# Optimization experiments

Hardware: AMD Instinct MI355X
Metric: run time of the kernel (lower is better)

Reference implementation:

```python
import jax, jax.numpy as jnp
import numpy as np

N = 100000      # nodes
E = 3200000     # edges (avg degree 32)
NFEAT = 512
HID = 64
NCLASS = 64
ALPHA = 0.1
NITER = 10


def setup_inputs() -> dict:
    key = jax.random.key(0)
    k1, k2, k3, k4, k5 = jax.random.split(key, 5)
    x = jax.random.normal(k1, (N, NFEAT), dtype=jnp.float32)
    edge_index = jax.random.randint(k2, (2, E), 0, N, dtype=jnp.int32)
    edge_weight = jax.random.uniform(k3, (E,), dtype=jnp.float32)
    W1 = jax.random.normal(k4, (NFEAT, HID), dtype=jnp.float32) * 0.05
    W2 = jax.random.normal(k5, (HID, NCLASS), dtype=jnp.float32) * 0.05
    return {"x": x, "edge_index": edge_index, "edge_weight": edge_weight,
            "W1": W1, "W2": W2}


def reference(x, edge_index, edge_weight, W1, W2):
    # _transform_features (eval mode: dropout = identity, bias=False)
    h = jax.nn.relu(x @ W1)            # [N, HID]
    z0 = h @ W2                        # [N, NCLASS]
    src = edge_index[0]
    dst = edge_index[1]
    z = z0
    # APPNP power iteration: z = adj @ z + alpha * z0
    for _ in range(NITER):
        msg = edge_weight[:, None] * z[src]                          # [E, NCLASS]
        z = jax.ops.segment_sum(msg, dst, num_segments=N) + ALPHA * z0
    return jax.nn.log_softmax(z, axis=-1)
```

## Files before the change

### kernel.cpp

```cpp
#include <hip/hip_runtime.h>

#define NN     100000
#define EE     3200000
#define NF     512
#define HIDN   64
#define NCLS   64
#define ALPHA  0.1f

#define CHUNK  512
#define NB     196

typedef unsigned short ushort_t;
typedef unsigned int   uint_t;

__device__ inline ushort_t f2bf(float f)
{
    uint_t u = __float_as_uint(f);
    u += 0x7FFFu + ((u >> 16) & 1u);
    return (ushort_t)(u >> 16);
}
__device__ inline float bf2f(ushort_t b)
{
    return __uint_as_float(((uint_t)b) << 16);
}

template <bool RELU>
__global__ __launch_bounds__(256) void gemm_kernel(
    const float* __restrict__ A, const float* __restrict__ B,
    float* __restrict__ C, int nrows, int K)
{
    const int BK = 16;
    __shared__ float AsT[BK][68];
    __shared__ float Bs [BK][68];

    int tid = threadIdx.x;
    int tx  = tid & 15;
    int ty  = tid >> 4;
    int rowBase = blockIdx.x * 64;

    int arow = tid >> 2;
    int ak   = (tid & 3) * 4;
    int brow = tid >> 4;
    int bcol = (tid & 15) * 4;

    float acc[4][4] = {};

    for (int k0 = 0; k0 < K; k0 += BK) {
        float4 av;
        int gr = rowBase + arow;
        if (gr < nrows) av = *(const float4*)(A + (size_t)gr * K + k0 + ak);
        else            av = make_float4(0.f, 0.f, 0.f, 0.f);
        float4 bv = *(const float4*)(B + (size_t)(k0 + brow) * 64 + bcol);

        __syncthreads();
        AsT[ak + 0][arow] = av.x;
        AsT[ak + 1][arow] = av.y;
        AsT[ak + 2][arow] = av.z;
        AsT[ak + 3][arow] = av.w;
        *(float4*)&Bs[brow][bcol] = bv;
        __syncthreads();

#pragma unroll
        for (int kk = 0; kk < BK; ++kk) {
            float4 a = *(const float4*)&AsT[kk][ty * 4];
            float4 b = *(const float4*)&Bs [kk][tx * 4];
            acc[0][0] = fmaf(a.x, b.x, acc[0][0]);
            acc[0][1] = fmaf(a.x, b.y, acc[0][1]);
            acc[0][2] = fmaf(a.x, b.z, acc[0][2]);
            acc[0][3] = fmaf(a.x, b.w, acc[0][3]);
            acc[1][0] = fmaf(a.y, b.x, acc[1][0]);
            acc[1][1] = fmaf(a.y, b.y, acc[1][1]);
            acc[1][2] = fmaf(a.y, b.z, acc[1][2]);
            acc[1][3] = fmaf(a.y, b.w, acc[1][3]);
            acc[2][0] = fmaf(a.z, b.x, acc[2][0]);
            acc[2][1] = fmaf(a.z, b.y, acc[2][1]);
            acc[2][2] = fmaf(a.z, b.z, acc[2][2]);
            acc[2][3] = fmaf(a.z, b.w, acc[2][3]);
            acc[3][0] = fmaf(a.w, b.x, acc[3][0]);
            acc[3][1] = fmaf(a.w, b.y, acc[3][1]);
            acc[3][2] = fmaf(a.w, b.z, acc[3][2]);
            acc[3][3] = fmaf(a.w, b.w, acc[3][3]);
        }
    }

#pragma unroll
    for (int i = 0; i < 4; ++i) {
        int r = rowBase + ty * 4 + i;
        if (r < nrows) {
            float4 o;
            o.x = acc[i][0]; o.y = acc[i][1]; o.z = acc[i][2]; o.w = acc[i][3];
            if (RELU) {
                o.x = fmaxf(o.x, 0.f); o.y = fmaxf(o.y, 0.f);
                o.z = fmaxf(o.z, 0.f); o.w = fmaxf(o.w, 0.f);
            }
            *(float4*)(C + (size_t)r * 64 + tx * 4) = o;
        }
    }
}

__global__ __launch_bounds__(256) void zero_kernel(int* __restrict__ p, int n)
{
    int i = blockIdx.x * 256 + threadIdx.x;
    if (i < n) p[i] = 0;
}

__global__ __launch_bounds__(256) void count_kernel(const int* __restrict__ dst,
                                                    int* __restrict__ deg)
{
    int e = blockIdx.x * 256 + threadIdx.x;
    if (e < EE) atomicAdd(&deg[dst[e]], 1);
}

__global__ __launch_bounds__(256) void scanA_kernel(const int* __restrict__ deg,
                                                    int* __restrict__ bsum)
{
    int b = blockIdx.x, t = threadIdx.x;
    int i = b * CHUNK + t * 2;
    int v = 0;
    if (i < NN)     v += deg[i];
    if (i + 1 < NN) v += deg[i + 1];
    __shared__ int sm[256];
    sm[t] = v;
    __syncthreads();
    for (int o = 128; o > 0; o >>= 1) {
        if (t < o) sm[t] += sm[t + o];
        __syncthreads();
    }
    if (t == 0) bsum[b] = sm[0];
}

__global__ __launch_bounds__(256) void scanB_kernel(const int* __restrict__ bsum,
                                                    int* __restrict__ bbase,
                                                    int* __restrict__ offs)
{
    int t = threadIdx.x;
    int v = (t < NB) ? bsum[t] : 0;
    __shared__ int sm[256];
    sm[t] = v;
    __syncthreads();
    for (int o = 1; o < 256; o <<= 1) {
        int u = (t >= o) ? sm[t - o] : 0;
        __syncthreads();
        sm[t] += u;
        __syncthreads();
    }
    if (t < NB) bbase[t] = sm[t] - v;
    if (t == 0) offs[NN] = EE;
}

__global__ __launch_bounds__(256) void scanC_kernel(const int* __restrict__ deg,
                                                    const int* __restrict__ bbase,
                                                    int* __restrict__ offs,
                                                    int* __restrict__ cursor)
{
    int b = blockIdx.x, t = threadIdx.x;
    int i0 = b * CHUNK + t * 2;
    int d0 = (i0 < NN)     ? deg[i0]     : 0;
    int d1 = (i0 + 1 < NN) ? deg[i0 + 1] : 0;
    int local = d0 + d1;
    __shared__ int sm[256];
    sm[t] = local;
    __syncthreads();
    for (int o = 1; o < 256; o <<= 1) {
        int u = (t >= o) ? sm[t - o] : 0;
        __syncthreads();
        sm[t] += u;
        __syncthreads();
    }
    int excl = sm[t] - local + bbase[b];
    if (i0 < NN)     { offs[i0]     = excl;      cursor[i0]     = excl;      }
    if (i0 + 1 < NN) { offs[i0 + 1] = excl + d0; cursor[i0 + 1] = excl + d0; }
}

__global__ __launch_bounds__(256) void scatter_kernel(
    const int* __restrict__ src, const int* __restrict__ dst,
    const float* __restrict__ w, int* cursor, int2* __restrict__ csr)
{
    int e = blockIdx.x * 256 + threadIdx.x;
    if (e >= EE) return;
    int d = dst[e];
    int pos = atomicAdd(&cursor[d], 1);
    csr[pos] = make_int2(src[e], __float_as_int(w[e]));
}

__global__ __launch_bounds__(256) void cvt_kernel(const float* __restrict__ z0,
                                                  ushort_t* __restrict__ zb)
{
    int i = (blockIdx.x * 256 + threadIdx.x) * 4;
    if (i >= NN * 64) return;
    float4 v = *(const float4*)(z0 + i);
    ushort4 o;
    o.x = f2bf(v.x); o.y = f2bf(v.y); o.z = f2bf(v.z); o.w = f2bf(v.w);
    *(ushort4*)(zb + i) = o;
}

template <bool LSM>
__global__ __launch_bounds__(256) void propagate_kernel(
    const ushort_t* __restrict__ zin, const float* __restrict__ z0,
    ushort_t* __restrict__ zout_b, float* __restrict__ zout_f,
    const int* __restrict__ offs, const int2* __restrict__ csr)
{
    int gid  = blockIdx.x * 256 + threadIdx.x;
    int node = gid >> 6;
    int lane = gid & 63;
    if (node >= NN) return;

    int beg = offs[node];
    int end = offs[node + 1];
    float acc = 0.f;
    int j = beg;
    for (; j + 8 <= end; j += 8) {
        int2 e0 = csr[j],     e1 = csr[j + 1], e2 = csr[j + 2], e3 = csr[j + 3];
        int2 e4 = csr[j + 4], e5 = csr[j + 5], e6 = csr[j + 6], e7 = csr[j + 7];
        float v0 = bf2f(zin[(size_t)e0.x * 64 + lane]);
        float v1 = bf2f(zin[(size_t)e1.x * 64 + lane]);
        float v2 = bf2f(zin[(size_t)e2.x * 64 + lane]);
        float v3 = bf2f(zin[(size_t)e3.x * 64 + lane]);
        float v4 = bf2f(zin[(size_t)e4.x * 64 + lane]);
        float v5 = bf2f(zin[(size_t)e5.x * 64 + lane]);
        float v6 = bf2f(zin[(size_t)e6.x * 64 + lane]);
        float v7 = bf2f(zin[(size_t)e7.x * 64 + lane]);
        acc = fmaf(__int_as_float(e0.y), v0, acc);
        acc = fmaf(__int_as_float(e1.y), v1, acc);
        acc = fmaf(__int_as_float(e2.y), v2, acc);
        acc = fmaf(__int_as_float(e3.y), v3, acc);
        acc = fmaf(__int_as_float(e4.y), v4, acc);
        acc = fmaf(__int_as_float(e5.y), v5, acc);
        acc = fmaf(__int_as_float(e6.y), v6, acc);
        acc = fmaf(__int_as_float(e7.y), v7, acc);
    }
    for (; j < end; ++j) {
        int2 e = csr[j];
        acc = fmaf(__int_as_float(e.y), bf2f(zin[(size_t)e.x * 64 + lane]), acc);
    }

    float out = fmaf(ALPHA, z0[(size_t)node * 64 + lane], acc);

    if (LSM) {
        float m = out;
#pragma unroll
        for (int o = 32; o > 0; o >>= 1) m = fmaxf(m, __shfl_xor(m, o, 64));
        float e = __expf(out - m);
        float s = e;
#pragma unroll
        for (int o = 32; o > 0; o >>= 1) s += __shfl_xor(s, o, 64);
        zout_f[(size_t)node * 64 + lane] = (out - m) - __logf(s);
    } else {
        zout_b[(size_t)node * 64 + lane] = f2bf(out);
    }
}

extern "C" void kernel_launch(void* const* d_in, const int* in_sizes, int n_in,
                              void* d_out, int out_size, void* d_ws, size_t ws_size,
                              hipStream_t stream)
{
    const float* x  = (const float*)d_in[0];
    const int*   ei = (const int*)  d_in[1];
    const float* ew = (const float*)d_in[2];
    const float* W1 = (const float*)d_in[3];
    const float* W2 = (const float*)d_in[4];
    const int* src = ei;
    const int* dst = ei + EE;

    char* ws = (char*)d_ws;
    size_t off = 0;
    auto alloc = [&](size_t bytes) -> char* {
        char* p = ws + off;
        off += (bytes + 255) & ~(size_t)255;
        return p;
    };

    float*    h     = (float*)   alloc((size_t)NN * HIDN * 4);
    float*    z0    = (float*)   alloc((size_t)NN * NCLS * 4);
    ushort_t* zbA   = (ushort_t*)alloc((size_t)NN * NCLS * 2);
    ushort_t* zbB   = (ushort_t*)alloc((size_t)NN * NCLS * 2);
    int*      deg   = (int*)     alloc((size_t)NN * 4);
    int*      offs  = (int*)     alloc((size_t)(NN + 1) * 4);
    int*      cur_  = (int*)     alloc((size_t)NN * 4);
    int*      bsum  = (int*)     alloc((size_t)NB * 4);
    int*      bbase = (int*)     alloc((size_t)NB * 4);

    int2* csr = (int2*)h;

    gemm_kernel<true ><<<(NN + 63) / 64, 256, 0, stream>>>(x, W1, h, NN, NF);
    gemm_kernel<false><<<(NN + 63) / 64, 256, 0, stream>>>(h, W2, z0, NN, HIDN);

    zero_kernel<<<(NN + 255) / 256, 256, 0, stream>>>(deg, NN);
    count_kernel<<<EE / 256, 256, 0, stream>>>(dst, deg);
    scanA_kernel<<<NB, 256, 0, stream>>>(deg, bsum);
    scanB_kernel<<<1, 256, 0, stream>>>(bsum, bbase, offs);
    scanC_kernel<<<NB, 256, 0, stream>>>(deg, bbase, offs, cur_);
    scatter_kernel<<<EE / 256, 256, 0, stream>>>(src, dst, ew, cur_, csr);

    cvt_kernel<<<(NN * 64 / 4 + 255) / 256, 256, 0, stream>>>(z0, zbA);

    const ushort_t* cur = zbA;
    ushort_t* nxt = zbB;
    for (int it = 0; it < 9; ++it) {
        propagate_kernel<false><<<(NN * 64) / 256, 256, 0, stream>>>(
            cur, z0, nxt, nullptr, offs, csr);
        ushort_t* t = (ushort_t*)cur; cur = nxt; nxt = t;
    }
    propagate_kernel<true><<<(NN * 64) / 256, 256, 0, stream>>>(
        cur, z0, nullptr, (float*)d_out, offs, csr);
}
```

Measured before the change: 1.610 ms.

## Fuse bf16 conversion into GEMM2, store alpha*z0 in bf16, partition scatter, nontemporal loads

The second GEMM now writes bf16 z0 and a precomputed bf16 alpha*z0 directly, which removes the separate conversion kernel and the fp32 z0 buffer. Each propagate pass therefore reads half the bytes for the residual term. The scatter kernel is restructured so each block handles one of 8 destination-node ranges, grouping atomics and CSR writes into smaller regions for locality. CSR edge loads and output stores use nontemporal hints. Rounding alpha*z0 to bf16 adds a little precision loss, and the scatter now reads dst eight times over.

```diff
diff --git a/kernel.cpp b/kernel.cpp
--- a/kernel.cpp
+++ b/kernel.cpp
@@ -10,6 +10,8 @@
 #define CHUNK  512
 #define NB     196
 
+#define SC_BLOCKS 2048
+
 typedef unsigned short ushort_t;
 typedef unsigned int   uint_t;
 
@@ -22,6 +24,16 @@
 __device__ inline float bf2f(ushort_t b)
 {
     return __uint_as_float(((uint_t)b) << 16);
+}
+
+__device__ inline int2 ldnt_e(const int2* p)
+{
+    unsigned long long v =
+        __builtin_nontemporal_load((const unsigned long long*)p);
+    int2 r;
+    r.x = (int)(v & 0xFFFFFFFFull);
+    r.y = (int)(v >> 32);
+    return r;
 }
 
 template <bool RELU>
@@ -98,6 +110,79 @@
     }
 }
 
+__global__ __launch_bounds__(256) void gemm2_kernel(
+    const float* __restrict__ A, const float* __restrict__ B,
+    ushort_t* __restrict__ zb, ushort_t* __restrict__ az, int nrows, int K)
+{
+    const int BK = 16;
+    __shared__ float AsT[BK][68];
+    __shared__ float Bs [BK][68];
+
+    int tid = threadIdx.x;
+    int tx  = tid & 15;
+    int ty  = tid >> 4;
+    int rowBase = blockIdx.x * 64;
+
+    int arow = tid >> 2;
+    int ak   = (tid & 3) * 4;
+    int brow = tid >> 4;
+    int bcol = (tid & 15) * 4;
+
+    float acc[4][4] = {};
+
+    for (int k0 = 0; k0 < K; k0 += BK) {
+        float4 av;
+        int gr = rowBase + arow;
+        if (gr < nrows) av = *(const float4*)(A + (size_t)gr * K + k0 + ak);
+        else            av = make_float4(0.f, 0.f, 0.f, 0.f);
+        float4 bv = *(const float4*)(B + (size_t)(k0 + brow) * 64 + bcol);
+
+        __syncthreads();
+        AsT[ak + 0][arow] = av.x;
+        AsT[ak + 1][arow] = av.y;
+        AsT[ak + 2][arow] = av.z;
+        AsT[ak + 3][arow] = av.w;
+        *(float4*)&Bs[brow][bcol] = bv;
+        __syncthreads();
+
+#pragma unroll
+        for (int kk = 0; kk < BK; ++kk) {
+            float4 a = *(const float4*)&AsT[kk][ty * 4];
+            float4 b = *(const float4*)&Bs [kk][tx * 4];
+            acc[0][0] = fmaf(a.x, b.x, acc[0][0]);
+            acc[0][1] = fmaf(a.x, b.y, acc[0][1]);
+            acc[0][2] = fmaf(a.x, b.z, acc[0][2]);
+            acc[0][3] = fmaf(a.x, b.w, acc[0][3]);
+            acc[1][0] = fmaf(a.y, b.x, acc[1][0]);
+            acc[1][1] = fmaf(a.y, b.y, acc[1][1]);
+            acc[1][2] = fmaf(a.y, b.z, acc[1][2]);
+            acc[1][3] = fmaf(a.y, b.w, acc[1][3]);
+            acc[2][0] = fmaf(a.z, b.x, acc[2][0]);
+            acc[2][1] = fmaf(a.z, b.y, acc[2][1]);
+            acc[2][2] = fmaf(a.z, b.z, acc[2][2]);
+            acc[2][3] = fmaf(a.z, b.w, acc[2][3]);
+            acc[3][0] = fmaf(a.w, b.x, acc[3][0]);
+            acc[3][1] = fmaf(a.w, b.y, acc[3][1]);
+            acc[3][2] = fmaf(a.w, b.z, acc[3][2]);
+            acc[3][3] = fmaf(a.w, b.w, acc[3][3]);
+        }
+    }
+
+#pragma unroll
+    for (int i = 0; i < 4; ++i) {
+        int r = rowBase + ty * 4 + i;
+        if (r < nrows) {
+            ushort4 o, oa;
+            o.x  = f2bf(acc[i][0]);         o.y  = f2bf(acc[i][1]);
+            o.z  = f2bf(acc[i][2]);         o.w  = f2bf(acc[i][3]);
+            oa.x = f2bf(ALPHA * acc[i][0]); oa.y = f2bf(ALPHA * acc[i][1]);
+            oa.z = f2bf(ALPHA * acc[i][2]); oa.w = f2bf(ALPHA * acc[i][3]);
+            *(ushort4*)(zb + (size_t)r * 64 + tx * 4) = o;
+            *(ushort4*)(az + (size_t)r * 64 + tx * 4) = oa;
+        }
+    }
+}
+
 __global__ __launch_bounds__(256) void zero_kernel(int* __restrict__ p, int n)
 {
     int i = blockIdx.x * 256 + threadIdx.x;
@@ -176,27 +261,23 @@
     const int* __restrict__ src, const int* __restrict__ dst,
     const float* __restrict__ w, int* cursor, int2* __restrict__ csr)
 {
-    int e = blockIdx.x * 256 + threadIdx.x;
-    if (e >= EE) return;
-    int d = dst[e];
-    int pos = atomicAdd(&cursor[d], 1);
-    csr[pos] = make_int2(src[e], __float_as_int(w[e]));
-}
-
-__global__ __launch_bounds__(256) void cvt_kernel(const float* __restrict__ z0,
-                                                  ushort_t* __restrict__ zb)
-{
-    int i = (blockIdx.x * 256 + threadIdx.x) * 4;
-    if (i >= NN * 64) return;
-    float4 v = *(const float4*)(z0 + i);
-    ushort4 o;
-    o.x = f2bf(v.x); o.y = f2bf(v.y); o.z = f2bf(v.z); o.w = f2bf(v.w);
-    *(ushort4*)(zb + i) = o;
+    const int x      = blockIdx.x & 7;
+    const int lo     = x * (NN / 8);
+    const int hi     = lo + (NN / 8);
+    const int nsl    = gridDim.x >> 3;
+    const int stride = nsl * 256;
+    for (int e = (blockIdx.x >> 3) * 256 + threadIdx.x; e < EE; e += stride) {
+        int d = dst[e];
+        if (d >= lo && d < hi) {
+            int pos = atomicAdd(&cursor[d], 1);
+            csr[pos] = make_int2(src[e], __float_as_int(w[e]));
+        }
+    }
 }
 
 template <bool LSM>
 __global__ __launch_bounds__(256) void propagate_kernel(
-    const ushort_t* __restrict__ zin, const float* __restrict__ z0,
+    const ushort_t* __restrict__ zin, const ushort_t* __restrict__ az0,
     ushort_t* __restrict__ zout_b, float* __restrict__ zout_f,
     const int* __restrict__ offs, const int2* __restrict__ csr)
 {
@@ -210,8 +291,10 @@
     float acc = 0.f;
     int j = beg;
     for (; j + 8 <= end; j += 8) {
-        int2 e0 = csr[j],     e1 = csr[j + 1], e2 = csr[j + 2], e3 = csr[j + 3];
-        int2 e4 = csr[j + 4], e5 = csr[j + 5], e6 = csr[j + 6], e7 = csr[j + 7];
+        int2 e0 = ldnt_e(csr + j);     int2 e1 = ldnt_e(csr + j + 1);
+        int2 e2 = ldnt_e(csr + j + 2); int2 e3 = ldnt_e(csr + j + 3);
+        int2 e4 = ldnt_e(csr + j + 4); int2 e5 = ldnt_e(csr + j + 5);
+        int2 e6 = ldnt_e(csr + j + 6); int2 e7 = ldnt_e(csr + j + 7);
         float v0 = bf2f(zin[(size_t)e0.x * 64 + lane]);
         float v1 = bf2f(zin[(size_t)e1.x * 64 + lane]);
         float v2 = bf2f(zin[(size_t)e2.x * 64 + lane]);
@@ -230,11 +313,11 @@
         acc = fmaf(__int_as_float(e7.y), v7, acc);
     }
     for (; j < end; ++j) {
-        int2 e = csr[j];
+        int2 e = ldnt_e(csr + j);
         acc = fmaf(__int_as_float(e.y), bf2f(zin[(size_t)e.x * 64 + lane]), acc);
     }
 
-    float out = fmaf(ALPHA, z0[(size_t)node * 64 + lane], acc);
+    float out = acc + bf2f(az0[(size_t)node * 64 + lane]);
 
     if (LSM) {
         float m = out;
@@ -244,9 +327,11 @@
         float s = e;
 #pragma unroll
         for (int o = 32; o > 0; o >>= 1) s += __shfl_xor(s, o, 64);
-        zout_f[(size_t)node * 64 + lane] = (out - m) - __logf(s);
+        __builtin_nontemporal_store((out - m) - __logf(s),
+                                    zout_f + (size_t)node * 64 + lane);
     } else {
-        zout_b[(size_t)node * 64 + lane] = f2bf(out);
+        __builtin_nontemporal_store(f2bf(out),
+                                    zout_b + (size_t)node * 64 + lane);
     }
 }
 
@@ -271,9 +356,9 @@
     };
 
     float*    h     = (float*)   alloc((size_t)NN * HIDN * 4);
-    float*    z0    = (float*)   alloc((size_t)NN * NCLS * 4);
     ushort_t* zbA   = (ushort_t*)alloc((size_t)NN * NCLS * 2);
     ushort_t* zbB   = (ushort_t*)alloc((size_t)NN * NCLS * 2);
+    ushort_t* az0   = (ushort_t*)alloc((size_t)NN * NCLS * 2);
     int*      deg   = (int*)     alloc((size_t)NN * 4);
     int*      offs  = (int*)     alloc((size_t)(NN + 1) * 4);
     int*      cur_  = (int*)     alloc((size_t)NN * 4);
@@ -282,25 +367,23 @@
 
     int2* csr = (int2*)h;
 
-    gemm_kernel<true ><<<(NN + 63) / 64, 256, 0, stream>>>(x, W1, h, NN, NF);
-    gemm_kernel<false><<<(NN + 63) / 64, 256, 0, stream>>>(h, W2, z0, NN, HIDN);
+    gemm_kernel<true><<<(NN + 63) / 64, 256, 0, stream>>>(x, W1, h, NN, NF);
+    gemm2_kernel<<<(NN + 63) / 64, 256, 0, stream>>>(h, W2, zbA, az0, NN, HIDN);
 
     zero_kernel<<<(NN + 255) / 256, 256, 0, stream>>>(deg, NN);
     count_kernel<<<EE / 256, 256, 0, stream>>>(dst, deg);
     scanA_kernel<<<NB, 256, 0, stream>>>(deg, bsum);
     scanB_kernel<<<1, 256, 0, stream>>>(bsum, bbase, offs);
     scanC_kernel<<<NB, 256, 0, stream>>>(deg, bbase, offs, cur_);
-    scatter_kernel<<<EE / 256, 256, 0, stream>>>(src, dst, ew, cur_, csr);
-
-    cvt_kernel<<<(NN * 64 / 4 + 255) / 256, 256, 0, stream>>>(z0, zbA);
+    scatter_kernel<<<SC_BLOCKS, 256, 0, stream>>>(src, dst, ew, cur_, csr);
 
     const ushort_t* cur = zbA;
     ushort_t* nxt = zbB;
     for (int it = 0; it < 9; ++it) {
         propagate_kernel<false><<<(NN * 64) / 256, 256, 0, stream>>>(
-            cur, z0, nxt, nullptr, offs, csr);
+            cur, az0, nxt, nullptr, offs, csr);
         ushort_t* t = (ushort_t*)cur; cur = nxt; nxt = t;
     }
     propagate_kernel<true><<<(NN * 64) / 256, 256, 0, stream>>>(
-        cur, z0, nullptr, (float*)d_out, offs, csr);
-}
+        cur, az0, nullptr, (float*)d_out, offs, csr);
+}
```

After: 1.885 ms. +17.0%, slower.
